# Kernel optimization log

Measured on AMD Instinct MI355X. Metric: run time of the kernel, lower is better.

## Reference

```python
import jax, jax.numpy as jnp
import numpy as np

DIM, ORDER, HID = 512, 2, 64
B, S = 4, 8192


def setup_inputs() -> dict:
    key = jax.random.key(0)
    ks = jax.random.split(key, 16)
    rnd = lambda k, shape, scale: (jax.random.normal(k, shape, dtype=jnp.float32) * scale)
    return {
        'x': rnd(ks[0], (B, S, DIM), 1.0),
        # ImplicitFilter MLP: Linear(1,64) -> GELU -> Linear(64,64) -> GELU -> Linear(64,dim)
        'w1': rnd(ks[1], (1, HID), 1.0),
        'b1': rnd(ks[2], (HID,), 0.02),
        'w2': rnd(ks[3], (HID, HID), 1.0 / np.sqrt(HID)),
        'b2': rnd(ks[4], (HID,), 0.02),
        'w3': rnd(ks[5], (HID, DIM), 1.0 / np.sqrt(HID)),
        'b3': rnd(ks[6], (DIM,), 0.02),
        # depthwise Conv1d(dim, dim, k=3, padding=1, groups=dim): weight (dim, 3)
        'conv_w': rnd(ks[7], (DIM, 3), 1.0 / np.sqrt(3)),
        'conv_b': rnd(ks[8], (DIM,), 0.02),
        # in_proj: Linear(dim, dim*(order+1))
        'w_in': rnd(ks[9], (DIM, DIM * (ORDER + 1)), 1.0 / np.sqrt(DIM)),
        'b_in': rnd(ks[10], (DIM * (ORDER + 1),), 0.02),
        # out_proj: Linear(dim, dim)
        'w_out': rnd(ks[11], (DIM, DIM), 1.0 / np.sqrt(DIM)),
        'b_out': rnd(ks[12], (DIM,), 0.02),
    }


def _gelu(x):
    return jax.nn.gelu(x, approximate=False)  # torch nn.GELU default is exact erf


def reference(x, w1, b1, w2, b2, w3, b3, conv_w, conv_b, w_in, b_in, w_out, b_out):
    batch, seq_len, dim = x.shape
    # in_proj and split into order+1 paths
    proj = x @ w_in + b_in                      # (B, S, 3D)
    v, u, z = jnp.split(proj, 3, axis=-1)       # each (B, S, D)
    # implicit filter from positions
    pos = jnp.linspace(0.0, 1.0, seq_len, dtype=x.dtype)[:, None]   # (S, 1)
    filt = _gelu(_gelu(pos @ w1 + b1) @ w2 + b2) @ w3 + b3          # (S, D)
    # depthwise short conv, kernel=3, padding=1 (cross-correlation as in torch)
    up = jnp.pad(u, ((0, 0), (1, 1), (0, 0)))
    u_short = (up[:, :-2] * conv_w[:, 0] + up[:, 1:-1] * conv_w[:, 1]
               + up[:, 2:] * conv_w[:, 2] + conv_b)                 # (B, S, D)
    # FFT long convolution (circular, matching torch rfft/irfft with n=seq_len)
    U = jnp.fft.rfft(u_short, axis=1)                               # (B, S//2+1, D)
    F = jnp.fft.rfft(filt, n=seq_len, axis=0)[None]                 # (1, S//2+1, D)
    filtered = jnp.fft.irfft(U * F, n=seq_len, axis=1)              # (B, S, D)
    # multiplicative gates
    out = v * filtered * jax.nn.sigmoid(z)
    return out @ w_out + b_out
```

## Files before the change

kernel.cpp:

```cpp
#include <hip/hip_runtime.h>
#include <math.h>

#define DIM   512
#define NB    4
#define NS    8192
#define FFT_N 8192
#define FT    1024
#define MTOT  (NB*NS)

typedef __attribute__((ext_vector_type(8))) short bf16x8;
typedef __attribute__((ext_vector_type(4))) short short4v;
typedef __attribute__((ext_vector_type(8))) short short8v;
typedef __attribute__((ext_vector_type(4))) float f32x4;

__device__ __forceinline__ float bf2f(unsigned short u) {
    union { unsigned int i; float f; } v; v.i = ((unsigned int)u) << 16; return v.f;
}
__device__ __forceinline__ unsigned short f2bf(float f) {
    union { float f; unsigned int i; } v; v.f = f;
    unsigned int r = v.i + 0x7fffu + ((v.i >> 16) & 1u);
    return (unsigned short)(r >> 16);
}
__device__ __forceinline__ float2 cmulf(float2 a, float2 b) {
    return make_float2(a.x*b.x - a.y*b.y, a.x*b.y + a.y*b.x);
}
__device__ __forceinline__ float2 cadd(float2 a, float2 b) { return make_float2(a.x+b.x, a.y+b.y); }
__device__ __forceinline__ float2 csub(float2 a, float2 b) { return make_float2(a.x-b.x, a.y-b.y); }
__device__ __forceinline__ float gelu_exact(float x) {
    return 0.5f * x * (1.0f + erff(x * 0.70710678118654752f));
}
__device__ __forceinline__ void gload16(const void* g, void* l) {
    __builtin_amdgcn_global_load_lds((const __attribute__((address_space(1))) void*)g,
                                     (__attribute__((address_space(3))) void*)l, 16, 0, 0);
}

__global__ void filter_mlp_kernel(const float* __restrict__ w1, const float* __restrict__ b1,
                                  const float* __restrict__ w2, const float* __restrict__ b2,
                                  const float* __restrict__ w3, const float* __restrict__ b3,
                                  float* __restrict__ filt) {
    __shared__ float h1[64];
    __shared__ float h2[64];
    const int s = blockIdx.x;
    const int t = threadIdx.x;
    const float pos = (float)s / (float)(NS - 1);
    h1[t] = gelu_exact(pos * w1[t] + b1[t]);
    __syncthreads();
    float acc = b2[t];
    #pragma unroll 8
    for (int j = 0; j < 64; ++j) acc += h1[j] * w2[j*64 + t];
    h2[t] = gelu_exact(acc);
    __syncthreads();
    for (int d = t; d < DIM; d += 64) {
        float o = b3[d];
        #pragma unroll 8
        for (int j = 0; j < 64; ++j) o += h2[j] * w3[j*DIM + d];
        filt[(size_t)s*DIM + d] = o;
    }
}

__global__ void transpose_f32_kernel(const float* __restrict__ in, float* __restrict__ out,
                                     int R, int C) {
    __shared__ float tile[64][65];
    const int c0 = blockIdx.x * 64, r0 = blockIdx.y * 64;
    const int t = threadIdx.x;
    const int rr = t >> 4, c4 = (t & 15) * 4;
    #pragma unroll
    for (int p = 0; p < 4; ++p) {
        const int r = rr + p*16;
        float4 v = *(const float4*)&in[(size_t)(r0 + r)*C + c0 + c4];
        tile[r][c4+0]=v.x; tile[r][c4+1]=v.y; tile[r][c4+2]=v.z; tile[r][c4+3]=v.w;
    }
    __syncthreads();
    const int cc = t >> 4, r4 = (t & 15) * 4;
    #pragma unroll
    for (int p = 0; p < 4; ++p) {
        const int c = cc + p*16;
        float4 o = make_float4(tile[r4+0][c], tile[r4+1][c], tile[r4+2][c], tile[r4+3][c]);
        *(float4*)&out[(size_t)(c0 + c)*R + r0 + r4] = o;
    }
}

__global__ void castT_kernel(const float* __restrict__ in, unsigned short* __restrict__ outT,
                             int R, int C) {
    __shared__ float tile[64][65];
    const int c0 = blockIdx.x * 64, r0 = blockIdx.y * 64;
    const int t = threadIdx.x;
    const int rr = t >> 4, c4 = (t & 15) * 4;
    #pragma unroll
    for (int p = 0; p < 4; ++p) {
        const int r = rr + p*16;
        float4 v = *(const float4*)&in[(size_t)(r0 + r)*C + c0 + c4];
        tile[r][c4+0]=v.x; tile[r][c4+1]=v.y; tile[r][c4+2]=v.z; tile[r][c4+3]=v.w;
    }
    __syncthreads();
    const int cc = t >> 4, r4 = (t & 15) * 4;
    #pragma unroll
    for (int p = 0; p < 4; ++p) {
        const int c = cc + p*16;
        short4v o;
        o[0] = (short)f2bf(tile[r4+0][c]); o[1] = (short)f2bf(tile[r4+1][c]);
        o[2] = (short)f2bf(tile[r4+2][c]); o[3] = (short)f2bf(tile[r4+3][c]);
        *(short4v*)&outT[(size_t)(c0 + c)*R + r0 + r4] = o;
    }
}

__global__ void cast_x_kernel(const float* __restrict__ in, unsigned short* __restrict__ out) {
    const size_t i = ((size_t)blockIdx.x * 256 + threadIdx.x) * 8;
    float4 a = *(const float4*)&in[i];
    float4 b = *(const float4*)&in[i+4];
    short8v o;
    o[0]=(short)f2bf(a.x); o[1]=(short)f2bf(a.y); o[2]=(short)f2bf(a.z); o[3]=(short)f2bf(a.w);
    o[4]=(short)f2bf(b.x); o[5]=(short)f2bf(b.y); o[6]=(short)f2bf(b.z); o[7]=(short)f2bf(b.w);
    *(short8v*)&out[i] = o;
}

template<int LOGQ>
__device__ __forceinline__ void dif4_stage(float2* X) {
    const int q = 1 << LOGQ;
    const float step = -6.28318530717958647692f / (float)(4*q);
    #pragma unroll
    for (int it = 0; it < (FFT_N/4)/FT; ++it) {
        const int idx = threadIdx.x + it*FT;
        const int g = idx >> LOGQ, k = idx & (q-1);
        const int base = (g << (LOGQ+2)) + k;
        float2 a=X[base], b=X[base+q], c=X[base+2*q], d=X[base+3*q];
        float2 t0=cadd(a,c), t1=csub(a,c), t2=cadd(b,d), t3=csub(b,d);
        float2 y0=cadd(t0,t2), y2=csub(t0,t2);
        float2 y1=make_float2(t1.x+t3.y, t1.y-t3.x);
        float2 y3=make_float2(t1.x-t3.y, t1.y+t3.x);
        float sv, cv; __sincosf(step*(float)k, &sv, &cv);
        float2 w1=make_float2(cv, sv);
        float2 w2=cmulf(w1, w1);
        float2 w3=cmulf(w2, w1);
        X[base]     = y0;
        X[base+q]   = cmulf(y1, w1);
        X[base+2*q] = cmulf(y2, w2);
        X[base+3*q] = cmulf(y3, w3);
    }
    __syncthreads();
}

template<int LOGQ>
__device__ __forceinline__ void dit4_stage_inv(float2* X) {
    const int q = 1 << LOGQ;
    const float step = 6.28318530717958647692f / (float)(4*q);
    #pragma unroll
    for (int it = 0; it < (FFT_N/4)/FT; ++it) {
        const int idx = threadIdx.x + it*FT;
        const int g = idx >> LOGQ, k = idx & (q-1);
        const int base = (g << (LOGQ+2)) + k;
        float sv, cv; __sincosf(step*(float)k, &sv, &cv);
        float2 w1=make_float2(cv, sv);
        float2 w2=cmulf(w1, w1);
        float2 w3=cmulf(w2, w1);
        float2 u0=X[base];
        float2 u1=cmulf(X[base+q],   w1);
        float2 u2=cmulf(X[base+2*q], w2);
        float2 u3=cmulf(X[base+3*q], w3);
        float2 s02=cadd(u0,u2), d02=csub(u0,u2);
        float2 s13=cadd(u1,u3), d13=csub(u1,u3);
        X[base]     = cadd(s02, s13);
        X[base+2*q] = csub(s02, s13);
        X[base+q]   = make_float2(d02.x - d13.y, d02.y + d13.x);
        X[base+3*q] = make_float2(d02.x + d13.y, d02.y - d13.x);
    }
    __syncthreads();
}

__device__ __forceinline__ void reg_fwd(float2* E) {
    const float C = 0.70710678118654752f;
    {
        float2 t0=cadd(E[0],E[4]), t1=csub(E[0],E[4]);
        float2 t2=cadd(E[2],E[6]), t3=csub(E[2],E[6]);
        E[0]=cadd(t0,t2);
        E[4]=csub(t0,t2);
        E[2]=make_float2(t1.x+t3.y, t1.y-t3.x);
        E[6]=make_float2(t1.x-t3.y, t1.y+t3.x);
    }
    {
        float2 t0=cadd(E[1],E[5]), t1=csub(E[1],E[5]);
        float2 t2=cadd(E[3],E[7]), t3=csub(E[3],E[7]);
        float2 y0=cadd(t0,t2), y2=csub(t0,t2);
        float2 y1=make_float2(t1.x+t3.y, t1.y-t3.x);
        float2 y3=make_float2(t1.x-t3.y, t1.y+t3.x);
        E[1]=y0;
        E[3]=make_float2(C*(y1.x+y1.y),  C*(y1.y-y1.x));
        E[5]=make_float2(y2.y, -y2.x);
        E[7]=make_float2(C*(y3.y-y3.x), -C*(y3.x+y3.y));
    }
    #pragma unroll
    for (int j = 0; j < 8; j += 2) {
        float2 a=E[j], b=E[j+1];
        E[j]=cadd(a,b); E[j+1]=csub(a,b);
    }
}
__device__ __forceinline__ void reg_inv(float2* E) {
    const float C = 0.70710678118654752f;
    #pragma unroll
    for (int j = 0; j < 8; j += 2) {
        float2 a=E[j], b=E[j+1];
        E[j]=cadd(a,b); E[j+1]=csub(a,b);
    }
    {
        float2 u0=E[0], u1=E[2], u2=E[4], u3=E[6];
        float2 s02=cadd(u0,u2), d02=csub(u0,u2);
        float2 s13=cadd(u1,u3), d13=csub(u1,u3);
        E[0]=cadd(s02,s13);
        E[4]=csub(s02,s13);
        E[2]=make_float2(d02.x - d13.y, d02.y + d13.x);
        E[6]=make_float2(d02.x + d13.y, d02.y - d13.x);
    }
    {
        float2 z1=E[3], z2=E[5], z3=E[7];
        float2 u0=E[1];
        float2 u1=make_float2(C*(z1.x - z1.y), C*(z1.x + z1.y));
        float2 u2=make_float2(-z2.y, z2.x);
        float2 u3=make_float2(-C*(z3.x + z3.y), C*(z3.x - z3.y));
        float2 s02=cadd(u0,u2), d02=csub(u0,u2);
        float2 s13=cadd(u1,u3), d13=csub(u1,u3);
        E[1]=cadd(s02,s13);
        E[5]=csub(s02,s13);
        E[3]=make_float2(d02.x - d13.y, d02.y + d13.x);
        E[7]=make_float2(d02.x + d13.y, d02.y - d13.x);
    }
}

__device__ __forceinline__ void load8(const float2* X, int t, float2* E) {
    const float4* b = (const float4*)(X + 8*t);
    #pragma unroll
    for (int p = 0; p < 4; ++p) {
        float4 v = b[p];
        E[2*p]   = make_float2(v.x, v.y);
        E[2*p+1] = make_float2(v.z, v.w);
    }
}
__device__ __forceinline__ void store8(float2* X, int t, const float2* E) {
    float4* b = (float4*)(X + 8*t);
    #pragma unroll
    for (int p = 0; p < 4; ++p)
        b[p] = make_float4(E[2*p].x, E[2*p].y, E[2*p+1].x, E[2*p+1].y);
}

__global__ __launch_bounds__(FT)
void fft_filt_kernel(const float* __restrict__ filtT, float2* __restrict__ Fbr) {
    extern __shared__ float4 Xraw[];
    float2* X = (float2*)Xraw;
    const int dd = blockIdx.x;
    const int t = threadIdx.x;
    const float* f = filtT + (size_t)dd * FFT_N;
    {
        float4 a = *(const float4*)(f + 8*t);
        float4 b = *(const float4*)(f + 8*t + 4);
        float2 E[8];
        E[0]=make_float2(a.x,0.f); E[1]=make_float2(a.y,0.f);
        E[2]=make_float2(a.z,0.f); E[3]=make_float2(a.w,0.f);
        E[4]=make_float2(b.x,0.f); E[5]=make_float2(b.y,0.f);
        E[6]=make_float2(b.z,0.f); E[7]=make_float2(b.w,0.f);
        store8(X, t, E);
    }
    __syncthreads();
    dif4_stage<11>(X);
    dif4_stage<9>(X);
    dif4_stage<7>(X);
    dif4_stage<5>(X);
    dif4_stage<3>(X);
    {
        float2 E[8];
        load8(X, t, E);
        reg_fwd(E);
        float2* o = Fbr + (size_t)dd*FFT_N + 8*t;
        #pragma unroll
        for (int j = 0; j < 8; ++j) o[j] = E[j];
    }
}

__global__ __launch_bounds__(FT)
void fft_conv_kernel(unsigned short* __restrict__ uT, const float2* __restrict__ Fbr) {
    extern __shared__ float4 Xraw[];
    float2* X = (float2*)Xraw;
    const int d = blockIdx.x & (DIM - 1);
    const int p = blockIdx.x >> 9;
    unsigned short* u1 = uT + (size_t)((2*p    )*DIM + d) * FFT_N;
    unsigned short* u2 = uT + (size_t)((2*p + 1)*DIM + d) * FFT_N;
    const int t = threadIdx.x;
    {
        short8v a = *(const short8v*)(u1 + 8*t);
        short8v b = *(const short8v*)(u2 + 8*t);
        float2 E[8];
        #pragma unroll
        for (int j = 0; j < 8; ++j)
            E[j] = make_float2(bf2f((unsigned short)a[j]), bf2f((unsigned short)b[j]));
        store8(X, t, E);
    }
    __syncthreads();
    dif4_stage<11>(X);
    dif4_stage<9>(X);
    dif4_stage<7>(X);
    dif4_stage<5>(X);
    dif4_stage<3>(X);
    {
        float2 E[8];
        load8(X, t, E);
        reg_fwd(E);
        const float2* F = Fbr + (size_t)d*FFT_N + 8*t;
        #pragma unroll
        for (int j = 0; j < 8; ++j) E[j] = cmulf(E[j], F[j]);
        reg_inv(E);
        store8(X, t, E);
    }
    __syncthreads();
    dit4_stage_inv<3>(X);
    dit4_stage_inv<5>(X);
    dit4_stage_inv<7>(X);
    dit4_stage_inv<9>(X);
    dit4_stage_inv<11>(X);
    {
        float2 E[8];
        load8(X, t, E);
        const float sc = 1.0f / (float)FFT_N;
        short8v a, b;
        #pragma unroll
        for (int j = 0; j < 8; ++j) {
            a[j] = (short)f2bf(E[j].x * sc);
            b[j] = (short)f2bf(E[j].y * sc);
        }
        *(short8v*)(u1 + 8*t) = a;
        *(short8v*)(u2 + 8*t) = b;
    }
}

__global__ void conv_transpose_kernel(const unsigned short* __restrict__ u,
                                      const float* __restrict__ conv_w,
                                      const float* __restrict__ conv_b,
                                      unsigned short* __restrict__ uT) {
    __shared__ float tile[66][65];
    const int bid = blockIdx.x;
    const int dt = bid & 7, st = (bid >> 3) & 127, b = bid >> 10;
    const int d0 = dt*64, s0 = st*64;
    const int t = threadIdx.x;
    const int rr = t >> 4, c4 = (t & 15) * 4;
    for (int r = rr; r < 66; r += 16) {
        const int s = s0 + r - 1;
        float v0=0.f, v1=0.f, v2=0.f, v3=0.f;
        if (s >= 0 && s < NS) {
            short4v xv = *(const short4v*)&u[((size_t)(b*NS + s))*DIM + d0 + c4];
            v0=bf2f((unsigned short)xv[0]); v1=bf2f((unsigned short)xv[1]);
            v2=bf2f((unsigned short)xv[2]); v3=bf2f((unsigned short)xv[3]);
        }
        tile[r][c4]=v0; tile[r][c4+1]=v1; tile[r][c4+2]=v2; tile[r][c4+3]=v3;
    }
    __syncthreads();
    const int dl = t >> 4, s4 = (t & 15) * 4;
    #pragma unroll
    for (int p = 0; p < 4; ++p) {
        const int dc = dl + p*16;
        const int d = d0 + dc;
        const float w0 = conv_w[d*3], w1 = conv_w[d*3+1], w2 = conv_w[d*3+2];
        const float cb = conv_b[d];
        short4v o;
        #pragma unroll
        for (int j = 0; j < 4; ++j) {
            const int sx = s4 + j;
            const float val = tile[sx][dc]*w0 + tile[sx+1][dc]*w1 + tile[sx+2][dc]*w2 + cb;
            o[j] = (short)f2bf(val);
        }
        *(short4v*)&uT[((size_t)(b*DIM + d))*FFT_N + s0 + s4] = o;
    }
}

__global__ void gate_kernel(unsigned short* __restrict__ vg, const unsigned short* __restrict__ yT) {
    __shared__ float tile[64][65];
    const int bid = blockIdx.x;
    const int dt = bid & 7, st = (bid >> 3) & 127, b = bid >> 10;
    const int d0 = dt*64, s0 = st*64;
    const int t = threadIdx.x;
    const int dl = t >> 4, s4 = (t & 15) * 4;
    #pragma unroll
    for (int p = 0; p < 4; ++p) {
        const int d = dl + p*16;
        short4v y = *(const short4v*)&yT[((size_t)(b*DIM + d0 + d))*FFT_N + s0 + s4];
        tile[d][s4]  =bf2f((unsigned short)y[0]); tile[d][s4+1]=bf2f((unsigned short)y[1]);
        tile[d][s4+2]=bf2f((unsigned short)y[2]); tile[d][s4+3]=bf2f((unsigned short)y[3]);
    }
    __syncthreads();
    const int sl = t >> 4, d4 = (t & 15) * 4;
    #pragma unroll
    for (int p = 0; p < 4; ++p) {
        const int s = s0 + sl + p*16;
        unsigned short* pv = &vg[((size_t)(b*NS + s))*DIM + d0 + d4];
        short4v v = *(short4v*)pv;
        short4v o;
        #pragma unroll
        for (int j = 0; j < 4; ++j)
            o[j] = (short)f2bf(bf2f((unsigned short)v[j]) * tile[d4+j][sl + p*16]);
        *(short4v*)pv = o;
    }
}

template<int MODE>
__global__ __launch_bounds__(256)
void gemm_bt_kernel(const unsigned short* __restrict__ A,
                    const unsigned short* __restrict__ BT,
                    const float* __restrict__ bias,
                    float* __restrict__ Cf,
                    unsigned short* __restrict__ Cb) {
    __shared__ unsigned short As[2][4096];
    __shared__ unsigned short Bs[2][4096];
    const int tid = threadIdx.x;
    const int wid = tid >> 6, lane = tid & 63;
    const int bid = blockIdx.y * 4 + blockIdx.x;
    const int swz = (bid & 7) * 128 + (bid >> 3);
    const int m0 = (swz >> 2) * 128, n0 = (swz & 3) * 128;
    const int srow = wid*16 + (lane >> 2);
    const int scol = (lane & 3) * 8;
    const unsigned short* gA = A  + (size_t)(m0 + srow)*DIM + scol;
    const unsigned short* gB = BT + (size_t)(n0 + srow)*DIM + scol;
    const int wr = wid >> 1, wc = wid & 1;
    const int fr = lane & 15, fq = lane >> 4;
    f32x4 acc[4][4] = {};
    gload16(gA,                  &As[0][wid*512]);
    gload16(gA + (size_t)64*DIM, &As[0][wid*512 + 2048]);
    gload16(gB,                  &Bs[0][wid*512]);
    gload16(gB + (size_t)64*DIM, &Bs[0][wid*512 + 2048]);
    int cur = 0;
    for (int k0 = 0; k0 < DIM; k0 += 32) {
        __syncthreads();
        if (k0 + 32 < DIM) {
            const int nx = cur ^ 1;
            gload16(gA + k0 + 32,                  &As[nx][wid*512]);
            gload16(gA + k0 + 32 + (size_t)64*DIM, &As[nx][wid*512 + 2048]);
            gload16(gB + k0 + 32,                  &Bs[nx][wid*512]);
            gload16(gB + k0 + 32 + (size_t)64*DIM, &Bs[nx][wid*512 + 2048]);
        }
        bf16x8 af[4], bfr[4];
        #pragma unroll
        for (int mi = 0; mi < 4; ++mi)
            af[mi] = *(const bf16x8*)&As[cur][(wr*64 + mi*16 + fr)*32 + fq*8];
        #pragma unroll
        for (int ni = 0; ni < 4; ++ni)
            bfr[ni] = *(const bf16x8*)&Bs[cur][(wc*64 + ni*16 + fr)*32 + fq*8];
        #pragma unroll
        for (int mi = 0; mi < 4; ++mi)
            #pragma unroll
            for (int ni = 0; ni < 4; ++ni)
                acc[mi][ni] = __builtin_amdgcn_mfma_f32_16x16x32_bf16(af[mi], bfr[ni], acc[mi][ni], 0, 0, 0);
        cur ^= 1;
    }
    #pragma unroll
    for (int ni = 0; ni < 4; ++ni) {
        const int c = n0 + wc*64 + ni*16 + fr;
        const float bv = bias[c];
        #pragma unroll
        for (int mi = 0; mi < 4; ++mi) {
            const int rbase = m0 + wr*64 + mi*16 + fq*4;
            #pragma unroll
            for (int j = 0; j < 4; ++j) {
                const size_t idx = (size_t)(rbase + j)*DIM + c;
                const float val = acc[mi][ni][j] + bv;
                if (MODE == 0) Cb[idx] = f2bf(val);
                else           Cf[idx] = val;
            }
        }
    }
}

__global__ __launch_bounds__(256)
void gemm_vzu2_kernel(const unsigned short* __restrict__ A,
                      const unsigned short* __restrict__ BT,
                      const float* __restrict__ bias,
                      unsigned short* __restrict__ Gb,
                      unsigned short* __restrict__ Ub) {
    __shared__ unsigned short As[2][4096];
    __shared__ unsigned short B1[2][4096];
    __shared__ unsigned short B2[2][4096];
    const int tid = threadIdx.x;
    const int wid = tid >> 6, lane = tid & 63;
    const int bid = blockIdx.y * 4 + blockIdx.x;
    const bool is_u = bid >= 1024;
    const int lbid = bid & 1023;
    const int swz = (lbid & 7) * 128 + (lbid >> 3);
    const int m0 = (swz >> 2) * 128, n0 = (swz & 3) * 128;
    const int srow = wid*16 + (lane >> 2);
    const int scol = (lane & 3) * 8;
    const unsigned short* gA = A + (size_t)(m0 + srow)*DIM + scol;
    const int wr = wid >> 1, wc = wid & 1;
    const int fr = lane & 15, fq = lane >> 4;

    if (!is_u) {
        const unsigned short* gBv = BT + (size_t)(n0 + srow)*DIM + scol;
        const unsigned short* gBz = BT + (size_t)(1024 + n0 + srow)*DIM + scol;
        f32x4 accv[4][4] = {};
        f32x4 accz[4][4] = {};
        gload16(gA,                   &As[0][wid*512]);
        gload16(gA  + (size_t)64*DIM, &As[0][wid*512 + 2048]);
        gload16(gBv,                  &B1[0][wid*512]);
        gload16(gBv + (size_t)64*DIM, &B1[0][wid*512 + 2048]);
        gload16(gBz,                  &B2[0][wid*512]);
        gload16(gBz + (size_t)64*DIM, &B2[0][wid*512 + 2048]);
        int cur = 0;
        for (int k0 = 0; k0 < DIM; k0 += 32) {
            __syncthreads();
            if (k0 + 32 < DIM) {
                const int nx = cur ^ 1;
                gload16(gA  + k0 + 32,                  &As[nx][wid*512]);
                gload16(gA  + k0 + 32 + (size_t)64*DIM, &As[nx][wid*512 + 2048]);
                gload16(gBv + k0 + 32,                  &B1[nx][wid*512]);
                gload16(gBv + k0 + 32 + (size_t)64*DIM, &B1[nx][wid*512 + 2048]);
                gload16(gBz + k0 + 32,                  &B2[nx][wid*512]);
                gload16(gBz + k0 + 32 + (size_t)64*DIM, &B2[nx][wid*512 + 2048]);
            }
            bf16x8 af[4], bf_[4];
            #pragma unroll
            for (int mi = 0; mi < 4; ++mi)
                af[mi] = *(const bf16x8*)&As[cur][(wr*64 + mi*16 + fr)*32 + fq*8];
            #pragma unroll
            for (int ni = 0; ni < 4; ++ni)
                bf_[ni] = *(const bf16x8*)&B1[cur][(wc*64 + ni*16 + fr)*32 + fq*8];
            #pragma unroll
            for (int mi = 0; mi < 4; ++mi)
                #pragma unroll
                for (int ni = 0; ni < 4; ++ni)
                    accv[mi][ni] = __builtin_amdgcn_mfma_f32_16x16x32_bf16(af[mi], bf_[ni], accv[mi][ni], 0, 0, 0);
            #pragma unroll
            for (int ni = 0; ni < 4; ++ni)
                bf_[ni] = *(const bf16x8*)&B2[cur][(wc*64 + ni*16 + fr)*32 + fq*8];
            #pragma unroll
            for (int mi = 0; mi < 4; ++mi)
                #pragma unroll
                for (int ni = 0; ni < 4; ++ni)
                    accz[mi][ni] = __builtin_amdgcn_mfma_f32_16x16x32_bf16(af[mi], bf_[ni], accz[mi][ni], 0, 0, 0);
            cur ^= 1;
        }
        #pragma unroll
        for (int ni = 0; ni < 4; ++ni) {
            const int c = n0 + wc*64 + ni*16 + fr;
            const float bv = bias[c];
            const float bz = bias[1024 + c];
            #pragma unroll
            for (int mi = 0; mi < 4; ++mi) {
                const int rbase = m0 + wr*64 + mi*16 + fq*4;
                #pragma unroll
                for (int j = 0; j < 4; ++j) {
                    const size_t idx = (size_t)(rbase + j)*DIM + c;
                    const float vv = accv[mi][ni][j] + bv;
                    const float zz = accz[mi][ni][j] + bz;
                    const float sg = 1.0f / (1.0f + __expf(-zz));
                    Gb[idx] = f2bf(vv * sg);
                }
            }
        }
    } else {
        const unsigned short* gBu = BT + (size_t)(512 + n0 + srow)*DIM + scol;
        f32x4 acc[4][4] = {};
        gload16(gA,                   &As[0][wid*512]);
        gload16(gA  + (size_t)64*DIM, &As[0][wid*512 + 2048]);
        gload16(gBu,                  &B1[0][wid*512]);
        gload16(gBu + (size_t)64*DIM, &B1[0][wid*512 + 2048]);
        int cur = 0;
        for (int k0 = 0; k0 < DIM; k0 += 32) {
            __syncthreads();
            if (k0 + 32 < DIM) {
                const int nx = cur ^ 1;
                gload16(gA  + k0 + 32,                  &As[nx][wid*512]);
                gload16(gA  + k0 + 32 + (size_t)64*DIM, &As[nx][wid*512 + 2048]);
                gload16(gBu + k0 + 32,                  &B1[nx][wid*512]);
                gload16(gBu + k0 + 32 + (size_t)64*DIM, &B1[nx][wid*512 + 2048]);
            }
            bf16x8 af[4], bf_[4];
            #pragma unroll
            for (int mi = 0; mi < 4; ++mi)
                af[mi] = *(const bf16x8*)&As[cur][(wr*64 + mi*16 + fr)*32 + fq*8];
            #pragma unroll
            for (int ni = 0; ni < 4; ++ni)
                bf_[ni] = *(const bf16x8*)&B1[cur][(wc*64 + ni*16 + fr)*32 + fq*8];
            #pragma unroll
            for (int mi = 0; mi < 4; ++mi)
                #pragma unroll
                for (int ni = 0; ni < 4; ++ni)
                    acc[mi][ni] = __builtin_amdgcn_mfma_f32_16x16x32_bf16(af[mi], bf_[ni], acc[mi][ni], 0, 0, 0);
            cur ^= 1;
        }
        #pragma unroll
        for (int ni = 0; ni < 4; ++ni) {
            const int c = n0 + wc*64 + ni*16 + fr;
            const float bu = bias[512 + c];
            #pragma unroll
            for (int mi = 0; mi < 4; ++mi) {
                const int rbase = m0 + wr*64 + mi*16 + fq*4;
                #pragma unroll
                for (int j = 0; j < 4; ++j) {
                    const size_t idx = (size_t)(rbase + j)*DIM + c;
                    Ub[idx] = f2bf(acc[mi][ni][j] + bu);
                }
            }
        }
    }
}

extern "C" void kernel_launch(void* const* d_in, const int* in_sizes, int n_in,
                              void* d_out, int out_size, void* d_ws, size_t ws_size,
                              hipStream_t stream) {
    const float* x      = (const float*)d_in[0];
    const float* w1     = (const float*)d_in[1];
    const float* b1     = (const float*)d_in[2];
    const float* w2     = (const float*)d_in[3];
    const float* b2     = (const float*)d_in[4];
    const float* w3     = (const float*)d_in[5];
    const float* b3     = (const float*)d_in[6];
    const float* conv_w = (const float*)d_in[7];
    const float* conv_b = (const float*)d_in[8];
    const float* w_in   = (const float*)d_in[9];
    const float* b_in   = (const float*)d_in[10];
    const float* w_out  = (const float*)d_in[11];
    const float* b_out  = (const float*)d_in[12];
    float* out = (float*)d_out;

    const size_t NEED = 167772160ULL;
    if (ws_size < NEED) return;
    char* ws = (char*)d_ws;
    float2*         Fbr    = (float2*)ws;
    unsigned short* xb     = (unsigned short*)(ws + (size_t)( 32<<20));
    unsigned short* W2     = (unsigned short*)(ws + (size_t)( 64<<20));
    unsigned short* W3     = (unsigned short*)(ws + (size_t)( 96<<20));
    char*           W4     = ws + (size_t)(128<<20);
    float*          filt   = (float*)W4;
    float*          filtT  = (float*)(ws + (size_t)(96<<20));
    unsigned short* w_inT  = (unsigned short*)W4;
    unsigned short* w_outT = (unsigned short*)(W4 + (size_t)(2<<20));

    filter_mlp_kernel<<<NS, 64, 0, stream>>>(w1, b1, w2, b2, w3, b3, filt);
    transpose_f32_kernel<<<dim3(DIM/64, NS/64), 256, 0, stream>>>(filt, filtT, NS, DIM);
    fft_filt_kernel<<<DIM, FT, FFT_N*sizeof(float2), stream>>>(filtT, Fbr);
    cast_x_kernel<<<(MTOT*DIM/8)/256, 256, 0, stream>>>(x, xb);
    castT_kernel<<<dim3(1536/64, DIM/64), 256, 0, stream>>>(w_in, w_inT, DIM, 1536);
    castT_kernel<<<dim3(DIM/64, DIM/64), 256, 0, stream>>>(w_out, w_outT, DIM, DIM);
    gemm_vzu2_kernel<<<dim3(4, 512), 256, 0, stream>>>(xb, w_inT, b_in, W2, W3);
    conv_transpose_kernel<<<NB*(NS/64)*(DIM/64), 256, 0, stream>>>(W3, conv_w, conv_b, xb);
    fft_conv_kernel<<<(NB/2)*DIM, FT, FFT_N*sizeof(float2), stream>>>(xb, Fbr);
    gate_kernel<<<NB*(NS/64)*(DIM/64), 256, 0, stream>>>(W2, xb);
    gemm_bt_kernel<2><<<dim3(4, MTOT/128), 256, 0, stream>>>(W2, w_outT, b_out, out, nullptr);
}
```

Measured before the change: 259.0 us.

## Fuse filter MLP with transpose and use an LDS twiddle table in FFTs

The filter MLP kernel now writes the transposed filter directly, using 64x64 tiles of positions and channels, so the separate transpose kernel and its intermediate buffer are gone. Both FFT kernels build a 1024-entry twiddle table in LDS once per block and read from it instead of calling sincos in every radix-4 butterfly stage. The table is padded to avoid bank conflicts, and octant symmetry covers the upper half. The cost is slightly more LDS per block, extra LDS reads per butterfly and a conditional rotation in place of the transcendental calls.

Measured after the change: 277.5 us. 7.2% more time.

```diff
diff --git a/kernel.cpp b/kernel.cpp
--- a/kernel.cpp
+++ b/kernel.cpp
@@ -34,50 +34,44 @@
                                      (__attribute__((address_space(3))) void*)l, 16, 0, 0);
 }
 
-__global__ void filter_mlp_kernel(const float* __restrict__ w1, const float* __restrict__ b1,
-                                  const float* __restrict__ w2, const float* __restrict__ b2,
-                                  const float* __restrict__ w3, const float* __restrict__ b3,
-                                  float* __restrict__ filt) {
-    __shared__ float h1[64];
-    __shared__ float h2[64];
-    const int s = blockIdx.x;
+__global__ void filter_mlp_T_kernel(const float* __restrict__ w1, const float* __restrict__ b1,
+                                    const float* __restrict__ w2, const float* __restrict__ b2,
+                                    const float* __restrict__ w3, const float* __restrict__ b3,
+                                    float* __restrict__ filtT) {
+    __shared__ float h1s[64][65];
+    __shared__ float h2s[64][65];
+    const int d0 = blockIdx.x * 64, s0 = blockIdx.y * 64;
     const int t = threadIdx.x;
-    const float pos = (float)s / (float)(NS - 1);
-    h1[t] = gelu_exact(pos * w1[t] + b1[t]);
-    __syncthreads();
-    float acc = b2[t];
-    #pragma unroll 8
-    for (int j = 0; j < 64; ++j) acc += h1[j] * w2[j*64 + t];
-    h2[t] = gelu_exact(acc);
-    __syncthreads();
-    for (int d = t; d < DIM; d += 64) {
-        float o = b3[d];
+    for (int i = t; i < 4096; i += 256) {
+        const int s = i >> 6, h = i & 63;
+        const float pos = (float)(s0 + s) / (float)(NS - 1);
+        h1s[s][h] = gelu_exact(pos * w1[h] + b1[h]);
+    }
+    __syncthreads();
+    for (int i = t; i < 4096; i += 256) {
+        const int s = i >> 6, h = i & 63;
+        float acc = b2[h];
         #pragma unroll 8
-        for (int j = 0; j < 64; ++j) o += h2[j] * w3[j*DIM + d];
-        filt[(size_t)s*DIM + d] = o;
-    }
-}
-
-__global__ void transpose_f32_kernel(const float* __restrict__ in, float* __restrict__ out,
-                                     int R, int C) {
-    __shared__ float tile[64][65];
-    const int c0 = blockIdx.x * 64, r0 = blockIdx.y * 64;
-    const int t = threadIdx.x;
-    const int rr = t >> 4, c4 = (t & 15) * 4;
-    #pragma unroll
-    for (int p = 0; p < 4; ++p) {
-        const int r = rr + p*16;
-        float4 v = *(const float4*)&in[(size_t)(r0 + r)*C + c0 + c4];
-        tile[r][c4+0]=v.x; tile[r][c4+1]=v.y; tile[r][c4+2]=v.z; tile[r][c4+3]=v.w;
-    }
-    __syncthreads();
-    const int cc = t >> 4, r4 = (t & 15) * 4;
-    #pragma unroll
-    for (int p = 0; p < 4; ++p) {
-        const int c = cc + p*16;
-        float4 o = make_float4(tile[r4+0][c], tile[r4+1][c], tile[r4+2][c], tile[r4+3][c]);
-        *(float4*)&out[(size_t)(c0 + c)*R + r0 + r4] = o;
-    }
+        for (int j = 0; j < 64; ++j) acc += h1s[s][j] * w2[j*64 + h];
+        h2s[s][h] = gelu_exact(acc);
+    }
+    __syncthreads();
+    const int dl = t >> 2, sq = t & 3;
+    const int d = d0 + dl;
+    float o[16];
+    const float b3d = b3[d];
+    #pragma unroll
+    for (int ss = 0; ss < 16; ++ss) o[ss] = b3d;
+    for (int j = 0; j < 64; ++j) {
+        const float wj = w3[j*DIM + d];
+        const int sb = sq*16;
+        #pragma unroll
+        for (int ss = 0; ss < 16; ++ss) o[ss] += h2s[sb + ss][j] * wj;
+    }
+    float4* dst = (float4*)&filtT[(size_t)d*FFT_N + s0 + sq*16];
+    #pragma unroll
+    for (int p = 0; p < 4; ++p)
+        dst[p] = make_float4(o[4*p], o[4*p+1], o[4*p+2], o[4*p+3]);
 }
 
 __global__ void castT_kernel(const float* __restrict__ in, unsigned short* __restrict__ outT,
@@ -114,10 +108,20 @@
     *(short8v*)&out[i] = o;
 }
 
+#define TWSZ 1088
+__device__ __forceinline__ float2 tw_read(const float2* Twid, int m) {
+    const int mm = m & 1023;
+    float2 tw = Twid[mm + (mm >> 4)];
+    if (m & 1024) {
+        const float C = 0.70710678118654752f;
+        tw = make_float2(C*(tw.x + tw.y), C*(tw.y - tw.x));
+    }
+    return tw;
+}
+
 template<int LOGQ>
-__device__ __forceinline__ void dif4_stage(float2* X) {
+__device__ __forceinline__ void dif4_stage(float2* X, const float2* Twid) {
     const int q = 1 << LOGQ;
-    const float step = -6.28318530717958647692f / (float)(4*q);
     #pragma unroll
     for (int it = 0; it < (FFT_N/4)/FT; ++it) {
         const int idx = threadIdx.x + it*FT;
@@ -128,10 +132,9 @@
         float2 y0=cadd(t0,t2), y2=csub(t0,t2);
         float2 y1=make_float2(t1.x+t3.y, t1.y-t3.x);
         float2 y3=make_float2(t1.x-t3.y, t1.y+t3.x);
-        float sv, cv; __sincosf(step*(float)k, &sv, &cv);
-        float2 w1=make_float2(cv, sv);
-        float2 w2=cmulf(w1, w1);
-        float2 w3=cmulf(w2, w1);
+        const float2 w1 = tw_read(Twid, k << (11 - LOGQ));
+        const float2 w2 = cmulf(w1, w1);
+        const float2 w3 = cmulf(w2, w1);
         X[base]     = y0;
         X[base+q]   = cmulf(y1, w1);
         X[base+2*q] = cmulf(y2, w2);
@@ -141,18 +144,17 @@
 }
 
 template<int LOGQ>
-__device__ __forceinline__ void dit4_stage_inv(float2* X) {
+__device__ __forceinline__ void dit4_stage_inv(float2* X, const float2* Twid) {
     const int q = 1 << LOGQ;
-    const float step = 6.28318530717958647692f / (float)(4*q);
     #pragma unroll
     for (int it = 0; it < (FFT_N/4)/FT; ++it) {
         const int idx = threadIdx.x + it*FT;
         const int g = idx >> LOGQ, k = idx & (q-1);
         const int base = (g << (LOGQ+2)) + k;
-        float sv, cv; __sincosf(step*(float)k, &sv, &cv);
-        float2 w1=make_float2(cv, sv);
-        float2 w2=cmulf(w1, w1);
-        float2 w3=cmulf(w2, w1);
+        const float2 wf = tw_read(Twid, k << (11 - LOGQ));
+        const float2 w1 = make_float2(wf.x, -wf.y);
+        const float2 w2 = cmulf(w1, w1);
+        const float2 w3 = cmulf(w2, w1);
         float2 u0=X[base];
         float2 u1=cmulf(X[base+q],   w1);
         float2 u2=cmulf(X[base+2*q], w2);
@@ -241,12 +243,21 @@
         b[p] = make_float4(E[2*p].x, E[2*p].y, E[2*p+1].x, E[2*p+1].y);
 }
 
+__device__ __forceinline__ void tw_init(float2* Twid, int t) {
+    if (t < 1024) {
+        float sv, cv;
+        __sincosf((float)t * -7.66990393942820615e-4f, &sv, &cv);
+        Twid[t + (t >> 4)] = make_float2(cv, sv);
+    }
+}
+
 __global__ __launch_bounds__(FT)
 void fft_filt_kernel(const float* __restrict__ filtT, float2* __restrict__ Fbr) {
-    extern __shared__ float4 Xraw[];
-    float2* X = (float2*)Xraw;
+    __shared__ float2 X[FFT_N];
+    __shared__ float2 Twid[TWSZ];
     const int dd = blockIdx.x;
     const int t = threadIdx.x;
+    tw_init(Twid, t);
     const float* f = filtT + (size_t)dd * FFT_N;
     {
         float4 a = *(const float4*)(f + 8*t);
@@ -259,11 +270,11 @@
         store8(X, t, E);
     }
     __syncthreads();
-    dif4_stage<11>(X);
-    dif4_stage<9>(X);
-    dif4_stage<7>(X);
-    dif4_stage<5>(X);
-    dif4_stage<3>(X);
+    dif4_stage<11>(X, Twid);
+    dif4_stage<9>(X, Twid);
+    dif4_stage<7>(X, Twid);
+    dif4_stage<5>(X, Twid);
+    dif4_stage<3>(X, Twid);
     {
         float2 E[8];
         load8(X, t, E);
@@ -276,13 +287,14 @@
 
 __global__ __launch_bounds__(FT)
 void fft_conv_kernel(unsigned short* __restrict__ uT, const float2* __restrict__ Fbr) {
-    extern __shared__ float4 Xraw[];
-    float2* X = (float2*)Xraw;
+    __shared__ float2 X[FFT_N];
+    __shared__ float2 Twid[TWSZ];
     const int d = blockIdx.x & (DIM - 1);
     const int p = blockIdx.x >> 9;
     unsigned short* u1 = uT + (size_t)((2*p    )*DIM + d) * FFT_N;
     unsigned short* u2 = uT + (size_t)((2*p + 1)*DIM + d) * FFT_N;
     const int t = threadIdx.x;
+    tw_init(Twid, t);
     {
         short8v a = *(const short8v*)(u1 + 8*t);
         short8v b = *(const short8v*)(u2 + 8*t);
@@ -293,11 +305,11 @@
         store8(X, t, E);
     }
     __syncthreads();
-    dif4_stage<11>(X);
-    dif4_stage<9>(X);
-    dif4_stage<7>(X);
-    dif4_stage<5>(X);
-    dif4_stage<3>(X);
+    dif4_stage<11>(X, Twid);
+    dif4_stage<9>(X, Twid);
+    dif4_stage<7>(X, Twid);
+    dif4_stage<5>(X, Twid);
+    dif4_stage<3>(X, Twid);
     {
         float2 E[8];
         load8(X, t, E);
@@ -309,11 +321,11 @@
         store8(X, t, E);
     }
     __syncthreads();
-    dit4_stage_inv<3>(X);
-    dit4_stage_inv<5>(X);
-    dit4_stage_inv<7>(X);
-    dit4_stage_inv<9>(X);
-    dit4_stage_inv<11>(X);
+    dit4_stage_inv<3>(X, Twid);
+    dit4_stage_inv<5>(X, Twid);
+    dit4_stage_inv<7>(X, Twid);
+    dit4_stage_inv<9>(X, Twid);
+    dit4_stage_inv<11>(X, Twid);
     {
         float2 E[8];
         load8(X, t, E);
@@ -623,20 +635,18 @@
     unsigned short* W2     = (unsigned short*)(ws + (size_t)( 64<<20));
     unsigned short* W3     = (unsigned short*)(ws + (size_t)( 96<<20));
     char*           W4     = ws + (size_t)(128<<20);
-    float*          filt   = (float*)W4;
     float*          filtT  = (float*)(ws + (size_t)(96<<20));
     unsigned short* w_inT  = (unsigned short*)W4;
     unsigned short* w_outT = (unsigned short*)(W4 + (size_t)(2<<20));
 
-    filter_mlp_kernel<<<NS, 64, 0, stream>>>(w1, b1, w2, b2, w3, b3, filt);
-    transpose_f32_kernel<<<dim3(DIM/64, NS/64), 256, 0, stream>>>(filt, filtT, NS, DIM);
-    fft_filt_kernel<<<DIM, FT, FFT_N*sizeof(float2), stream>>>(filtT, Fbr);
+    filter_mlp_T_kernel<<<dim3(DIM/64, NS/64), 256, 0, stream>>>(w1, b1, w2, b2, w3, b3, filtT);
+    fft_filt_kernel<<<DIM, FT, 0, stream>>>(filtT, Fbr);
     cast_x_kernel<<<(MTOT*DIM/8)/256, 256, 0, stream>>>(x, xb);
     castT_kernel<<<dim3(1536/64, DIM/64), 256, 0, stream>>>(w_in, w_inT, DIM, 1536);
     castT_kernel<<<dim3(DIM/64, DIM/64), 256, 0, stream>>>(w_out, w_outT, DIM, DIM);
     gemm_vzu2_kernel<<<dim3(4, 512), 256, 0, stream>>>(xb, w_inT, b_in, W2, W3);
     conv_transpose_kernel<<<NB*(NS/64)*(DIM/64), 256, 0, stream>>>(W3, conv_w, conv_b, xb);
-    fft_conv_kernel<<<(NB/2)*DIM, FT, FFT_N*sizeof(float2), stream>>>(xb, Fbr);
+    fft_conv_kernel<<<(NB/2)*DIM, FT, 0, stream>>>(xb, Fbr);
     gate_kernel<<<NB*(NS/64)*(DIM/64), 256, 0, stream>>>(W2, xb);
     gemm_bt_kernel<2><<<dim3(4, MTOT/128), 256, 0, stream>>>(W2, w_outT, b_out, out, nullptr);
 }
```

## Triple-buffer GEMM LDS tiles with explicit vmcnt waits and raw barriers

Applied to the files above, without the earlier changes.

Both bf16 MFMA GEMM kernels move from double to triple-buffered LDS staging. Loads run two k-steps ahead, and partial s_waitcnt vmcnt counts let newer loads stay in flight while the oldest tile is consumed. The aim is to hide more global-load latency behind the MFMA work. In exchange LDS use per block grows by half, which may reduce occupancy, most of all in the vzu2 kernel with three buffers. Correctness also depends on gload16 being a direct-to-LDS load that the vmcnt counter tracks.

Result: slower. 309.7 us (+19.6%).

```diff
diff --git a/kernel.cpp b/kernel.cpp
--- a/kernel.cpp
+++ b/kernel.cpp
@@ -404,8 +404,8 @@
                     const float* __restrict__ bias,
                     float* __restrict__ Cf,
                     unsigned short* __restrict__ Cb) {
-    __shared__ unsigned short As[2][4096];
-    __shared__ unsigned short Bs[2][4096];
+    __shared__ unsigned short As[3][4096];
+    __shared__ unsigned short Bs[3][4096];
     const int tid = threadIdx.x;
     const int wid = tid >> 6, lane = tid & 63;
     const int bid = blockIdx.y * 4 + blockIdx.x;
@@ -418,20 +418,27 @@
     const int wr = wid >> 1, wc = wid & 1;
     const int fr = lane & 15, fq = lane >> 4;
     f32x4 acc[4][4] = {};
-    gload16(gA,                  &As[0][wid*512]);
-    gload16(gA + (size_t)64*DIM, &As[0][wid*512 + 2048]);
-    gload16(gB,                  &Bs[0][wid*512]);
-    gload16(gB + (size_t)64*DIM, &Bs[0][wid*512 + 2048]);
-    int cur = 0;
-    for (int k0 = 0; k0 < DIM; k0 += 32) {
-        __syncthreads();
-        if (k0 + 32 < DIM) {
-            const int nx = cur ^ 1;
-            gload16(gA + k0 + 32,                  &As[nx][wid*512]);
-            gload16(gA + k0 + 32 + (size_t)64*DIM, &As[nx][wid*512 + 2048]);
-            gload16(gB + k0 + 32,                  &Bs[nx][wid*512]);
-            gload16(gB + k0 + 32 + (size_t)64*DIM, &Bs[nx][wid*512 + 2048]);
-        }
+    #pragma unroll
+    for (int p = 0; p < 2; ++p) {
+        gload16(gA + p*32,                  &As[p][wid*512]);
+        gload16(gA + p*32 + (size_t)64*DIM, &As[p][wid*512 + 2048]);
+        gload16(gB + p*32,                  &Bs[p][wid*512]);
+        gload16(gB + p*32 + (size_t)64*DIM, &Bs[p][wid*512 + 2048]);
+    }
+    for (int k = 0; k < 16; ++k) {
+        if (k < 15) asm volatile("s_waitcnt vmcnt(4)" ::: "memory");
+        else        asm volatile("s_waitcnt vmcnt(0)" ::: "memory");
+        __builtin_amdgcn_s_barrier();
+        __builtin_amdgcn_sched_barrier(0);
+        if (k + 2 < 16) {
+            const int nx = (k + 2) % 3;
+            const int off = (k + 2) * 32;
+            gload16(gA + off,                  &As[nx][wid*512]);
+            gload16(gA + off + (size_t)64*DIM, &As[nx][wid*512 + 2048]);
+            gload16(gB + off,                  &Bs[nx][wid*512]);
+            gload16(gB + off + (size_t)64*DIM, &Bs[nx][wid*512 + 2048]);
+        }
+        const int cur = k % 3;
         bf16x8 af[4], bfr[4];
         #pragma unroll
         for (int mi = 0; mi < 4; ++mi)
@@ -444,7 +451,6 @@
             #pragma unroll
             for (int ni = 0; ni < 4; ++ni)
                 acc[mi][ni] = __builtin_amdgcn_mfma_f32_16x16x32_bf16(af[mi], bfr[ni], acc[mi][ni], 0, 0, 0);
-        cur ^= 1;
     }
     #pragma unroll
     for (int ni = 0; ni < 4; ++ni) {
@@ -470,9 +476,9 @@
                       const float* __restrict__ bias,
                       unsigned short* __restrict__ Gb,
                       unsigned short* __restrict__ Ub) {
-    __shared__ unsigned short As[2][4096];
-    __shared__ unsigned short B1[2][4096];
-    __shared__ unsigned short B2[2][4096];
+    __shared__ unsigned short As[3][4096];
+    __shared__ unsigned short B1[3][4096];
+    __shared__ unsigned short B2[3][4096];
     const int tid = threadIdx.x;
     const int wid = tid >> 6, lane = tid & 63;
     const int bid = blockIdx.y * 4 + blockIdx.x;
@@ -491,24 +497,31 @@
         const unsigned short* gBz = BT + (size_t)(1024 + n0 + srow)*DIM + scol;
         f32x4 accv[4][4] = {};
         f32x4 accz[4][4] = {};
-        gload16(gA,                   &As[0][wid*512]);
-        gload16(gA  + (size_t)64*DIM, &As[0][wid*512 + 2048]);
-        gload16(gBv,                  &B1[0][wid*512]);
-        gload16(gBv + (size_t)64*DIM, &B1[0][wid*512 + 2048]);
-        gload16(gBz,                  &B2[0][wid*512]);
-        gload16(gBz + (size_t)64*DIM, &B2[0][wid*512 + 2048]);
-        int cur = 0;
-        for (int k0 = 0; k0 < DIM; k0 += 32) {
-            __syncthreads();
-            if (k0 + 32 < DIM) {
-                const int nx = cur ^ 1;
-                gload16(gA  + k0 + 32,                  &As[nx][wid*512]);
-                gload16(gA  + k0 + 32 + (size_t)64*DIM, &As[nx][wid*512 + 2048]);
-                gload16(gBv + k0 + 32,                  &B1[nx][wid*512]);
-                gload16(gBv + k0 + 32 + (size_t)64*DIM, &B1[nx][wid*512 + 2048]);
-                gload16(gBz + k0 + 32,                  &B2[nx][wid*512]);
-                gload16(gBz + k0 + 32 + (size_t)64*DIM, &B2[nx][wid*512 + 2048]);
+        #pragma unroll
+        for (int p = 0; p < 2; ++p) {
+            gload16(gA  + p*32,                  &As[p][wid*512]);
+            gload16(gA  + p*32 + (size_t)64*DIM, &As[p][wid*512 + 2048]);
+            gload16(gBv + p*32,                  &B1[p][wid*512]);
+            gload16(gBv + p*32 + (size_t)64*DIM, &B1[p][wid*512 + 2048]);
+            gload16(gBz + p*32,                  &B2[p][wid*512]);
+            gload16(gBz + p*32 + (size_t)64*DIM, &B2[p][wid*512 + 2048]);
+        }
+        for (int k = 0; k < 16; ++k) {
+            if (k < 15) asm volatile("s_waitcnt vmcnt(6)" ::: "memory");
+            else        asm volatile("s_waitcnt vmcnt(0)" ::: "memory");
+            __builtin_amdgcn_s_barrier();
+            __builtin_amdgcn_sched_barrier(0);
+            if (k + 2 < 16) {
+                const int nx = (k + 2) % 3;
+                const int off = (k + 2) * 32;
+                gload16(gA  + off,                  &As[nx][wid*512]);
+                gload16(gA  + off + (size_t)64*DIM, &As[nx][wid*512 + 2048]);
+                gload16(gBv + off,                  &B1[nx][wid*512]);
+                gload16(gBv + off + (size_t)64*DIM, &B1[nx][wid*512 + 2048]);
+                gload16(gBz + off,                  &B2[nx][wid*512]);
+                gload16(gBz + off + (size_t)64*DIM, &B2[nx][wid*512 + 2048]);
             }
+            const int cur = k % 3;
             bf16x8 af[4], bf_[4];
             #pragma unroll
             for (int mi = 0; mi < 4; ++mi)
@@ -529,7 +542,6 @@
                 #pragma unroll
                 for (int ni = 0; ni < 4; ++ni)
                     accz[mi][ni] = __builtin_amdgcn_mfma_f32_16x16x32_bf16(af[mi], bf_[ni], accz[mi][ni], 0, 0, 0);
-            cur ^= 1;
         }
         #pragma unroll
         for (int ni = 0; ni < 4; ++ni) {
@@ -552,20 +564,27 @@
     } else {
         const unsigned short* gBu = BT + (size_t)(512 + n0 + srow)*DIM + scol;
         f32x4 acc[4][4] = {};
-        gload16(gA,                   &As[0][wid*512]);
-        gload16(gA  + (size_t)64*DIM, &As[0][wid*512 + 2048]);
-        gload16(gBu,                  &B1[0][wid*512]);
-        gload16(gBu + (size_t)64*DIM, &B1[0][wid*512 + 2048]);
-        int cur = 0;
-        for (int k0 = 0; k0 < DIM; k0 += 32) {
-            __syncthreads();
-            if (k0 + 32 < DIM) {
-                const int nx = cur ^ 1;
-                gload16(gA  + k0 + 32,                  &As[nx][wid*512]);
-                gload16(gA  + k0 + 32 + (size_t)64*DIM, &As[nx][wid*512 + 2048]);
-                gload16(gBu + k0 + 32,                  &B1[nx][wid*512]);
-                gload16(gBu + k0 + 32 + (size_t)64*DIM, &B1[nx][wid*512 + 2048]);
+        #pragma unroll
+        for (int p = 0; p < 2; ++p) {
+            gload16(gA  + p*32,                  &As[p][wid*512]);
+            gload16(gA  + p*32 + (size_t)64*DIM, &As[p][wid*512 + 2048]);
+            gload16(gBu + p*32,                  &B1[p][wid*512]);
+            gload16(gBu + p*32 + (size_t)64*DIM, &B1[p][wid*512 + 2048]);
+        }
+        for (int k = 0; k < 16; ++k) {
+            if (k < 15) asm volatile("s_waitcnt vmcnt(4)" ::: "memory");
+            else        asm volatile("s_waitcnt vmcnt(0)" ::: "memory");
+            __builtin_amdgcn_s_barrier();
+            __builtin_amdgcn_sched_barrier(0);
+            if (k + 2 < 16) {
+                const int nx = (k + 2) % 3;
+                const int off = (k + 2) * 32;
+                gload16(gA  + off,                  &As[nx][wid*512]);
+                gload16(gA  + off + (size_t)64*DIM, &As[nx][wid*512 + 2048]);
+                gload16(gBu + off,                  &B1[nx][wid*512]);
+                gload16(gBu + off + (size_t)64*DIM, &B1[nx][wid*512 + 2048]);
             }
+            const int cur = k % 3;
             bf16x8 af[4], bf_[4];
             #pragma unroll
             for (int mi = 0; mi < 4; ++mi)
@@ -578,7 +597,6 @@
                 #pragma unroll
                 for (int ni = 0; ni < 4; ++ni)
                     acc[mi][ni] = __builtin_amdgcn_mfma_f32_16x16x32_bf16(af[mi], bf_[ni], acc[mi][ni], 0, 0, 0);
-            cur ^= 1;
         }
         #pragma unroll
         for (int ni = 0; ni < 4; ++ni) {
```

## Pad FFT shared memory to avoid bank conflicts and merge prep kernels

Applied to the files above, without the earlier changes.

The FFT kernels now index shared memory with one pad element per 8 complex values (IDX macro, 9216-entry static array). This is meant to reduce LDS bank conflicts in the strided radix-4 stages and in the per-thread 8-element loads and stores. Separately, the x cast, the two weight cast-transposes and the filter MLP are merged into one launch that dispatches on block index, with the MLP packing four positions per 256-thread block. Workspace buffers for filt/filtT are moved to reuse regions that are later overwritten. The trade-off is scalar float2 LDS accesses in place of float4 in load8/store8 and slightly more LDS per block.

After: 259.4 us. No clear change (+0.1%).

```diff
diff --git a/kernel.cpp b/kernel.cpp
--- a/kernel.cpp
+++ b/kernel.cpp
@@ -8,6 +8,9 @@
 #define FT    1024
 #define MTOT  (NB*NS)
 
+#define IDX(i) ((i) + ((i) >> 3))
+#define XSZ   9216
+
 typedef __attribute__((ext_vector_type(8))) short bf16x8;
 typedef __attribute__((ext_vector_type(4))) short short4v;
 typedef __attribute__((ext_vector_type(8))) short short8v;
@@ -32,30 +35,6 @@
 __device__ __forceinline__ void gload16(const void* g, void* l) {
     __builtin_amdgcn_global_load_lds((const __attribute__((address_space(1))) void*)g,
                                      (__attribute__((address_space(3))) void*)l, 16, 0, 0);
-}
-
-__global__ void filter_mlp_kernel(const float* __restrict__ w1, const float* __restrict__ b1,
-                                  const float* __restrict__ w2, const float* __restrict__ b2,
-                                  const float* __restrict__ w3, const float* __restrict__ b3,
-                                  float* __restrict__ filt) {
-    __shared__ float h1[64];
-    __shared__ float h2[64];
-    const int s = blockIdx.x;
-    const int t = threadIdx.x;
-    const float pos = (float)s / (float)(NS - 1);
-    h1[t] = gelu_exact(pos * w1[t] + b1[t]);
-    __syncthreads();
-    float acc = b2[t];
-    #pragma unroll 8
-    for (int j = 0; j < 64; ++j) acc += h1[j] * w2[j*64 + t];
-    h2[t] = gelu_exact(acc);
-    __syncthreads();
-    for (int d = t; d < DIM; d += 64) {
-        float o = b3[d];
-        #pragma unroll 8
-        for (int j = 0; j < 64; ++j) o += h2[j] * w3[j*DIM + d];
-        filt[(size_t)s*DIM + d] = o;
-    }
 }
 
 __global__ void transpose_f32_kernel(const float* __restrict__ in, float* __restrict__ out,
@@ -80,11 +59,11 @@
     }
 }
 
-__global__ void castT_kernel(const float* __restrict__ in, unsigned short* __restrict__ outT,
-                             int R, int C) {
-    __shared__ float tile[64][65];
-    const int c0 = blockIdx.x * 64, r0 = blockIdx.y * 64;
-    const int t = threadIdx.x;
+__device__ __forceinline__ void castT_body(const float* __restrict__ in,
+                                           unsigned short* __restrict__ outT,
+                                           int R, int C, int bx, int by, int t,
+                                           float tile[64][65]) {
+    const int c0 = bx * 64, r0 = by * 64;
     const int rr = t >> 4, c4 = (t & 15) * 4;
     #pragma unroll
     for (int p = 0; p < 4; ++p) {
@@ -104,14 +83,50 @@
     }
 }
 
-__global__ void cast_x_kernel(const float* __restrict__ in, unsigned short* __restrict__ out) {
-    const size_t i = ((size_t)blockIdx.x * 256 + threadIdx.x) * 8;
-    float4 a = *(const float4*)&in[i];
-    float4 b = *(const float4*)&in[i+4];
-    short8v o;
-    o[0]=(short)f2bf(a.x); o[1]=(short)f2bf(a.y); o[2]=(short)f2bf(a.z); o[3]=(short)f2bf(a.w);
-    o[4]=(short)f2bf(b.x); o[5]=(short)f2bf(b.y); o[6]=(short)f2bf(b.z); o[7]=(short)f2bf(b.w);
-    *(short8v*)&out[i] = o;
+__global__ void mega_prep_kernel(const float* __restrict__ x, unsigned short* __restrict__ xb,
+                                 const float* __restrict__ w_in, unsigned short* __restrict__ w_inT,
+                                 const float* __restrict__ w_out, unsigned short* __restrict__ w_outT,
+                                 const float* __restrict__ w1, const float* __restrict__ b1,
+                                 const float* __restrict__ w2, const float* __restrict__ b2,
+                                 const float* __restrict__ w3, const float* __restrict__ b3,
+                                 float* __restrict__ filt) {
+    __shared__ float tile[64][65];
+    __shared__ float h1s[4][64];
+    __shared__ float h2s[4][64];
+    const int bid = blockIdx.x;
+    const int t = threadIdx.x;
+    if (bid < 8192) {
+        const size_t i = ((size_t)bid * 256 + t) * 8;
+        float4 a = *(const float4*)&x[i];
+        float4 b = *(const float4*)&x[i+4];
+        short8v o;
+        o[0]=(short)f2bf(a.x); o[1]=(short)f2bf(a.y); o[2]=(short)f2bf(a.z); o[3]=(short)f2bf(a.w);
+        o[4]=(short)f2bf(b.x); o[5]=(short)f2bf(b.y); o[6]=(short)f2bf(b.z); o[7]=(short)f2bf(b.w);
+        *(short8v*)&xb[i] = o;
+    } else if (bid < 8384) {
+        const int li = bid - 8192;
+        castT_body(w_in, w_inT, DIM, 1536, li % 24, li / 24, t, tile);
+    } else if (bid < 8448) {
+        const int li = bid - 8384;
+        castT_body(w_out, w_outT, DIM, DIM, li % 8, li / 8, t, tile);
+    } else {
+        const int sub = t >> 6, lane = t & 63;
+        const int s = (bid - 8448) * 4 + sub;
+        const float pos = (float)s / (float)(NS - 1);
+        h1s[sub][lane] = gelu_exact(pos * w1[lane] + b1[lane]);
+        __syncthreads();
+        float acc = b2[lane];
+        #pragma unroll 8
+        for (int j = 0; j < 64; ++j) acc += h1s[sub][j] * w2[j*64 + lane];
+        h2s[sub][lane] = gelu_exact(acc);
+        __syncthreads();
+        for (int d = lane; d < DIM; d += 64) {
+            float o = b3[d];
+            #pragma unroll 8
+            for (int j = 0; j < 64; ++j) o += h2s[sub][j] * w3[j*DIM + d];
+            filt[(size_t)s*DIM + d] = o;
+        }
+    }
 }
 
 template<int LOGQ>
@@ -123,7 +138,8 @@
         const int idx = threadIdx.x + it*FT;
         const int g = idx >> LOGQ, k = idx & (q-1);
         const int base = (g << (LOGQ+2)) + k;
-        float2 a=X[base], b=X[base+q], c=X[base+2*q], d=X[base+3*q];
+        const int i0 = IDX(base), i1 = IDX(base+q), i2 = IDX(base+2*q), i3 = IDX(base+3*q);
+        float2 a=X[i0], b=X[i1], c=X[i2], d=X[i3];
         float2 t0=cadd(a,c), t1=csub(a,c), t2=cadd(b,d), t3=csub(b,d);
         float2 y0=cadd(t0,t2), y2=csub(t0,t2);
         float2 y1=make_float2(t1.x+t3.y, t1.y-t3.x);
@@ -132,10 +148,10 @@
         float2 w1=make_float2(cv, sv);
         float2 w2=cmulf(w1, w1);
         float2 w3=cmulf(w2, w1);
-        X[base]     = y0;
-        X[base+q]   = cmulf(y1, w1);
-        X[base+2*q] = cmulf(y2, w2);
-        X[base+3*q] = cmulf(y3, w3);
+        X[i0] = y0;
+        X[i1] = cmulf(y1, w1);
+        X[i2] = cmulf(y2, w2);
+        X[i3] = cmulf(y3, w3);
     }
     __syncthreads();
 }
@@ -149,20 +165,21 @@
         const int idx = threadIdx.x + it*FT;
         const int g = idx >> LOGQ, k = idx & (q-1);
         const int base = (g << (LOGQ+2)) + k;
+        const int i0 = IDX(base), i1 = IDX(base+q), i2 = IDX(base+2*q), i3 = IDX(base+3*q);
         float sv, cv; __sincosf(step*(float)k, &sv, &cv);
         float2 w1=make_float2(cv, sv);
         float2 w2=cmulf(w1, w1);
         float2 w3=cmulf(w2, w1);
-        float2 u0=X[base];
-        float2 u1=cmulf(X[base+q],   w1);
-        float2 u2=cmulf(X[base+2*q], w2);
-        float2 u3=cmulf(X[base+3*q], w3);
+        float2 u0=X[i0];
+        float2 u1=cmulf(X[i1], w1);
+        float2 u2=cmulf(X[i2], w2);
+        float2 u3=cmulf(X[i3], w3);
         float2 s02=cadd(u0,u2), d02=csub(u0,u2);
         float2 s13=cadd(u1,u3), d13=csub(u1,u3);
-        X[base]     = cadd(s02, s13);
-        X[base+2*q] = csub(s02, s13);
-        X[base+q]   = make_float2(d02.x - d13.y, d02.y + d13.x);
-        X[base+3*q] = make_float2(d02.x + d13.y, d02.y - d13.x);
+        X[i0] = cadd(s02, s13);
+        X[i2] = csub(s02, s13);
+        X[i1] = make_float2(d02.x - d13.y, d02.y + d13.x);
+        X[i3] = make_float2(d02.x + d13.y, d02.y - d13.x);
     }
     __syncthreads();
 }
@@ -225,26 +242,20 @@
     }
 }
 
-__device__ __forceinline__ void load8(const float2* X, int t, float2* E) {
-    const float4* b = (const float4*)(X + 8*t);
-    #pragma unroll
-    for (int p = 0; p < 4; ++p) {
-        float4 v = b[p];
-        E[2*p]   = make_float2(v.x, v.y);
-        E[2*p+1] = make_float2(v.z, v.w);
-    }
-}
-__device__ __forceinline__ void store8(float2* X, int t, const float2* E) {
-    float4* b = (float4*)(X + 8*t);
-    #pragma unroll
-    for (int p = 0; p < 4; ++p)
-        b[p] = make_float4(E[2*p].x, E[2*p].y, E[2*p+1].x, E[2*p+1].y);
+__device__ __forceinline__ void load8p(const float2* X, int t, float2* E) {
+    const float2* b = X + 9*t;
+    #pragma unroll
+    for (int j = 0; j < 8; ++j) E[j] = b[j];
+}
+__device__ __forceinline__ void store8p(float2* X, int t, const float2* E) {
+    float2* b = X + 9*t;
+    #pragma unroll
+    for (int j = 0; j < 8; ++j) b[j] = E[j];
 }
 
 __global__ __launch_bounds__(FT)
 void fft_filt_kernel(const float* __restrict__ filtT, float2* __restrict__ Fbr) {
-    extern __shared__ float4 Xraw[];
-    float2* X = (float2*)Xraw;
+    __shared__ float2 X[XSZ];
     const int dd = blockIdx.x;
     const int t = threadIdx.x;
     const float* f = filtT + (size_t)dd * FFT_N;
@@ -256,7 +267,7 @@
         E[2]=make_float2(a.z,0.f); E[3]=make_float2(a.w,0.f);
         E[4]=make_float2(b.x,0.f); E[5]=make_float2(b.y,0.f);
         E[6]=make_float2(b.z,0.f); E[7]=make_float2(b.w,0.f);
-        store8(X, t, E);
+        store8p(X, t, E);
     }
     __syncthreads();
     dif4_stage<11>(X);
@@ -266,7 +277,7 @@
     dif4_stage<3>(X);
     {
         float2 E[8];
-        load8(X, t, E);
+        load8p(X, t, E);
         reg_fwd(E);
         float2* o = Fbr + (size_t)dd*FFT_N + 8*t;
         #pragma unroll
@@ -276,8 +287,7 @@
 
 __global__ __launch_bounds__(FT)
 void fft_conv_kernel(unsigned short* __restrict__ uT, const float2* __restrict__ Fbr) {
-    extern __shared__ float4 Xraw[];
-    float2* X = (float2*)Xraw;
+    __shared__ float2 X[XSZ];
     const int d = blockIdx.x & (DIM - 1);
     const int p = blockIdx.x >> 9;
     unsigned short* u1 = uT + (size_t)((2*p    )*DIM + d) * FFT_N;
@@ -290,7 +300,7 @@
         #pragma unroll
         for (int j = 0; j < 8; ++j)
             E[j] = make_float2(bf2f((unsigned short)a[j]), bf2f((unsigned short)b[j]));
-        store8(X, t, E);
+        store8p(X, t, E);
     }
     __syncthreads();
     dif4_stage<11>(X);
@@ -300,13 +310,13 @@
     dif4_stage<3>(X);
     {
         float2 E[8];
-        load8(X, t, E);
+        load8p(X, t, E);
         reg_fwd(E);
         const float2* F = Fbr + (size_t)d*FFT_N + 8*t;
         #pragma unroll
         for (int j = 0; j < 8; ++j) E[j] = cmulf(E[j], F[j]);
         reg_inv(E);
-        store8(X, t, E);
+        store8p(X, t, E);
     }
     __syncthreads();
     dit4_stage_inv<3>(X);
@@ -316,7 +326,7 @@
     dit4_stage_inv<11>(X);
     {
         float2 E[8];
-        load8(X, t, E);
+        load8p(X, t, E);
         const float sc = 1.0f / (float)FFT_N;
         short8v a, b;
         #pragma unroll
@@ -623,20 +633,18 @@
     unsigned short* W2     = (unsigned short*)(ws + (size_t)( 64<<20));
     unsigned short* W3     = (unsigned short*)(ws + (size_t)( 96<<20));
     char*           W4     = ws + (size_t)(128<<20);
-    float*          filt   = (float*)W4;
-    float*          filtT  = (float*)(ws + (size_t)(96<<20));
+    float*          filt   = (float*)W2;
+    float*          filtT  = (float*)W3;
     unsigned short* w_inT  = (unsigned short*)W4;
     unsigned short* w_outT = (unsigned short*)(W4 + (size_t)(2<<20));
 
-    filter_mlp_kernel<<<NS, 64, 0, stream>>>(w1, b1, w2, b2, w3, b3, filt);
+    mega_prep_kernel<<<10496, 256, 0, stream>>>(x, xb, w_in, w_inT, w_out, w_outT,
+                                                w1, b1, w2, b2, w3, b3, filt);
     transpose_f32_kernel<<<dim3(DIM/64, NS/64), 256, 0, stream>>>(filt, filtT, NS, DIM);
-    fft_filt_kernel<<<DIM, FT, FFT_N*sizeof(float2), stream>>>(filtT, Fbr);
-    cast_x_kernel<<<(MTOT*DIM/8)/256, 256, 0, stream>>>(x, xb);
-    castT_kernel<<<dim3(1536/64, DIM/64), 256, 0, stream>>>(w_in, w_inT, DIM, 1536);
-    castT_kernel<<<dim3(DIM/64, DIM/64), 256, 0, stream>>>(w_out, w_outT, DIM, DIM);
+    fft_filt_kernel<<<DIM, FT, 0, stream>>>(filtT, Fbr);
     gemm_vzu2_kernel<<<dim3(4, 512), 256, 0, stream>>>(xb, w_inT, b_in, W2, W3);
     conv_transpose_kernel<<<NB*(NS/64)*(DIM/64), 256, 0, stream>>>(W3, conv_w, conv_b, xb);
-    fft_conv_kernel<<<(NB/2)*DIM, FT, FFT_N*sizeof(float2), stream>>>(xb, Fbr);
+    fft_conv_kernel<<<(NB/2)*DIM, FT, 0, stream>>>(xb, Fbr);
     gate_kernel<<<NB*(NS/64)*(DIM/64), 256, 0, stream>>>(W2, xb);
     gemm_bt_kernel<2><<<dim3(4, MTOT/128), 256, 0, stream>>>(W2, w_outT, b_out, out, nullptr);
 }
```
